# Kernel tuning notes

Measured on AMD Instinct MI355X. Metric: run time of the kernel, lower is better.

The kernel has to match this reference:

```python
import jax, jax.numpy as jnp
import numpy as np

N_EMBD = 2048
H_I = 16   # indexer heads
D_I = 32   # indexer dim


def setup_inputs() -> dict:
    key = jax.random.key(0)
    k1, k2, k3, k4 = jax.random.split(key, 4)
    x = jax.random.normal(k1, (2, 4096, N_EMBD), dtype=jnp.float32)
    # nn.Linear(in, out, bias=False) weights, stored (out, in) like torch
    s = 1.0 / np.sqrt(N_EMBD)
    Wq = jax.random.uniform(k2, (H_I * D_I, N_EMBD), jnp.float32, -s, s)
    Wk = jax.random.uniform(k3, (D_I, N_EMBD), jnp.float32, -s, s)
    Ww = jax.random.uniform(k4, (H_I, N_EMBD), jnp.float32, -s, s)
    return {"x": x, "Wq": Wq, "Wk": Wk, "Ww": Ww}


def reference(x, Wq, Wk, Ww):
    B, T, C = x.shape
    q = (x @ Wq.T).reshape(B, T, H_I, D_I)   # (B,T,H,D)
    k = x @ Wk.T                              # (B,T,D)
    w = x @ Ww.T                              # (B,T,H)
    scores = jnp.einsum('bqhd,bkd->bqhk', q, k)
    scores = jax.nn.relu(scores)
    importance = jnp.einsum('bqh,bqhk->bqk', w, scores)  # (B,T,T)
    return importance
```

## Files before the change

kernel.cpp:

```cpp
#include <hip/hip_runtime.h>
#include <hip/hip_bf16.h>
#include <stdint.h>


typedef __attribute__((ext_vector_type(8))) short bf16x8;
typedef __attribute__((ext_vector_type(4))) float f32x4;
typedef __attribute__((ext_vector_type(2))) __fp16 f16x2;

__device__ __forceinline__ unsigned short f2bf(float f) {
  union { float f; unsigned u; } c; c.f = f;
  unsigned u = c.u;
  u += 0x7FFFu + ((u >> 16) & 1u);
  return (unsigned short)(u >> 16);
}

__device__ __forceinline__ f16x2 u32_to_h2(unsigned u) {
  union { unsigned u; f16x2 h; } c; c.u = u; return c.h;
}
__device__ __forceinline__ unsigned h2_to_u32(f16x2 h) {
  union { unsigned u; f16x2 h; } c; c.h = h; return c.u;
}

__device__ __forceinline__ void async_copy16(void* lds, const void* g) {
  __builtin_amdgcn_global_load_lds(
      (const __attribute__((address_space(1))) unsigned*)g,
      (__attribute__((address_space(3))) unsigned*)lds, 16, 0, 0);
}

__global__ __launch_bounds__(256) void pack_kernel(
    const float* __restrict__ x, const float* __restrict__ Wq,
    const float* __restrict__ Wk, const float* __restrict__ Ww,
    unsigned short* __restrict__ xb, unsigned short* __restrict__ Wp) {
  const int64_t NX4 = 16777216 / 4;
  int64_t i = (int64_t)blockIdx.x * 256 + threadIdx.x;
  if (i < NX4) {
    float4 v = ((const float4*)x)[i];
    ushort4 o;
    o.x = f2bf(v.x); o.y = f2bf(v.y); o.z = f2bf(v.z); o.w = f2bf(v.w);
    ((ushort4*)xb)[i] = o;
  } else {
    int p = (int)(i - NX4);
    int row = p >> 9;
    int col = (p & 511) << 2;
    float4 v = make_float4(0.f, 0.f, 0.f, 0.f);
    if (row < 512)      v = *(const float4*)(Wq + (int64_t)row * 2048 + col);
    else if (row < 544) v = *(const float4*)(Wk + (int64_t)(row - 512) * 2048 + col);
    else if (row < 560) v = *(const float4*)(Ww + (int64_t)(row - 544) * 2048 + col);
    ushort4 o;
    o.x = f2bf(v.x); o.y = f2bf(v.y); o.z = f2bf(v.z); o.w = f2bf(v.w);
    ((ushort4*)Wp)[p] = o;
  }
}

__global__ __launch_bounds__(256) void gemm_proj(
    const unsigned short* __restrict__ xb, const unsigned short* __restrict__ Wp,
    unsigned short* __restrict__ qh, unsigned short* __restrict__ kh,
    float* __restrict__ wf) {
  __shared__ short lds_a[2][64 * 64];
  __shared__ short lds_b[2][128 * 64];
  const int tid = threadIdx.x;
  const int lane = tid & 63;
  const int l15 = lane & 15, quad = lane >> 4;
  const int wave = tid >> 6;
  const int wn = wave;
  const int m0 = blockIdx.y * 64, n0 = blockIdx.x * 128;

  f32x4 acc[4][2] = {};

#define STAGE_A(buf, ko)                                                        \
  {                                                                             \
    _Pragma("unroll") for (int cc = 0; cc < 2; ++cc) {                          \
      int c = tid + cc * 256;                                                   \
      async_copy16(&lds_a[buf][c * 8],                                          \
                   xb + (int64_t)(m0 + (c >> 3)) * 2048 + (ko) + (c & 7) * 8);  \
    }                                                                           \
  }
#define STAGE_B(buf, ko)                                                        \
  {                                                                             \
    _Pragma("unroll") for (int cc = 0; cc < 4; ++cc) {                          \
      int c = tid + cc * 256;                                                   \
      async_copy16(&lds_b[buf][c * 8],                                          \
                   Wp + (int64_t)(n0 + (c >> 3)) * 2048 + (ko) + (c & 7) * 8);  \
    }                                                                           \
  }

  STAGE_A(0, 0);
  STAGE_B(0, 0);
  __syncthreads();

  for (int kt = 0; kt < 32; ++kt) {
    const int cur = kt & 1, nxt = cur ^ 1;
    if (kt < 31) {
      STAGE_A(nxt, (kt + 1) * 64);
      STAGE_B(nxt, (kt + 1) * 64);
    }
    bf16x8 af[4][2], bfr[2][2];
#pragma unroll
    for (int i = 0; i < 4; ++i)
#pragma unroll
      for (int s = 0; s < 2; ++s)
        af[i][s] = *(const bf16x8*)&lds_a[cur][(i * 16 + l15) * 64 + s * 32 + quad * 8];
#pragma unroll
    for (int j = 0; j < 2; ++j)
#pragma unroll
      for (int s = 0; s < 2; ++s)
        bfr[j][s] = *(const bf16x8*)&lds_b[cur][(wn * 32 + j * 16 + l15) * 64 + s * 32 + quad * 8];
#pragma unroll
    for (int s = 0; s < 2; ++s)
#pragma unroll
      for (int i = 0; i < 4; ++i)
#pragma unroll
        for (int j = 0; j < 2; ++j)
          acc[i][j] = __builtin_amdgcn_mfma_f32_16x16x32_bf16(af[i][s], bfr[j][s], acc[i][j], 0, 0, 0);
    __syncthreads();
  }
#undef STAGE_A
#undef STAGE_B

#pragma unroll
  for (int i = 0; i < 4; ++i)
#pragma unroll
    for (int j = 0; j < 2; ++j)
#pragma unroll
      for (int r = 0; r < 4; ++r) {
        int m = m0 + i * 16 + quad * 4 + r;
        int n = n0 + wn * 32 + j * 16 + l15;
        float v = acc[i][j][r];
        if (n < 512)      qh[((int64_t)(n >> 5) * 8192 + m) * 32 + (n & 31)] = f2bf(v);
        else if (n < 544) kh[(int64_t)m * 32 + (n - 512)] = f2bf(v);
        else if (n < 560) wf[m * 16 + (n - 544)] = v;
      }
}

__global__ __launch_bounds__(256) void scores_kernel(
    const unsigned short* __restrict__ qh, const unsigned short* __restrict__ kh,
    const float* __restrict__ wf, float* __restrict__ out) {
  const int kt = blockIdx.x, qt = blockIdx.y, b = blockIdx.z;
  const int tid = threadIdx.x;
  const int lane = tid & 63;
  const int l15 = lane & 15, quad = lane >> 4;
  const int wave = tid >> 6;
  const int wk = wave & 1, wq = wave >> 1;

  __shared__ unsigned w2[8][132];

  const int qrow0 = b * 4096 + qt * 128;
  const int krow0 = b * 4096 + kt * 128;

  {
    const float4* ws = (const float4*)(wf + (int64_t)qrow0 * 16);
#pragma unroll
    for (int r = 0; r < 2; ++r) {
      int f = tid * 2 + r;
      float4 v = ws[f];
      int row = f >> 2, hb = (f & 3) * 4;
      f16x2 p01, p23;
      p01.x = (__fp16)v.x; p01.y = (__fp16)v.y;
      p23.x = (__fp16)v.z; p23.y = (__fp16)v.w;
      w2[(hb >> 1) + 0][row] = h2_to_u32(p01);
      w2[(hb >> 1) + 1][row] = h2_to_u32(p23);
    }
  }

  bf16x8 ka[4];
#pragma unroll
  for (int i = 0; i < 4; ++i) {
    int kk = krow0 + wk * 64 + i * 16 + l15;
    ka[i] = *(const bf16x8*)&kh[(int64_t)kk * 32 + quad * 8];
  }

  const unsigned short* qbase =
      qh + (int64_t)(qrow0 + wq * 64 + l15) * 32 + quad * 8;

  f32x4 acc[4][4] = {};
  __syncthreads();

  const f16x2 hz = u32_to_h2(0u);
  const f32x4 z = {0.f, 0.f, 0.f, 0.f};

#pragma unroll
  for (int hp = 0; hp < 8; ++hp) {
    bf16x8 q0[4], q1[4];
#pragma unroll
    for (int j = 0; j < 4; ++j) {
      q0[j] = *(const bf16x8*)&qbase[(int64_t)(2 * hp) * 262144 + j * 512];
      q1[j] = *(const bf16x8*)&qbase[(int64_t)(2 * hp + 1) * 262144 + j * 512];
    }
    f16x2 wv[4];
#pragma unroll
    for (int j = 0; j < 4; ++j)
      wv[j] = u32_to_h2(w2[hp][wq * 64 + j * 16 + l15]);

#pragma unroll
    for (int i = 0; i < 4; ++i)
#pragma unroll
      for (int j = 0; j < 4; ++j) {
        f32x4 t0 = __builtin_amdgcn_mfma_f32_16x16x32_bf16(ka[i], q0[j], z, 0, 0, 0);
        f32x4 t1 = __builtin_amdgcn_mfma_f32_16x16x32_bf16(ka[i], q1[j], z, 0, 0, 0);
#pragma unroll
        for (int r = 0; r < 4; ++r) {
          f16x2 p = __builtin_amdgcn_cvt_pkrtz(t0[r], t1[r]);
          p = __builtin_elementwise_max(p, hz);
          acc[i][j][r] = __builtin_amdgcn_fdot2(p, wv[j], acc[i][j][r], false);
        }
      }
  }

#pragma unroll
  for (int i = 0; i < 4; ++i)
#pragma unroll
    for (int j = 0; j < 4; ++j) {
      int q = qt * 128 + wq * 64 + j * 16 + l15;
      int k = kt * 128 + wk * 64 + i * 16 + quad * 4;
      float4 v = make_float4(acc[i][j][0], acc[i][j][1], acc[i][j][2], acc[i][j][3]);
      *(float4*)&out[((int64_t)b * 4096 + q) * 4096 + k] = v;
    }
}

extern "C" void kernel_launch(void* const* d_in, const int* in_sizes, int n_in,
                              void* d_out, int out_size, void* d_ws, size_t ws_size,
                              hipStream_t stream) {
  const float* x  = (const float*)d_in[0];
  const float* Wq = (const float*)d_in[1];
  const float* Wk = (const float*)d_in[2];
  const float* Ww = (const float*)d_in[3];
  float* out = (float*)d_out;

  char* ws = (char*)d_ws;
  unsigned short* xb = (unsigned short*)ws;
  unsigned short* Wp = (unsigned short*)(ws + 33554432);
  unsigned short* qh = (unsigned short*)(ws + 36175872);
  unsigned short* kh = (unsigned short*)(ws + 44564480);
  float*          wf = (float*)(ws + 45088768);

  pack_kernel<<<17664, 256, 0, stream>>>(x, Wq, Wk, Ww, xb, Wp);
  gemm_proj<<<dim3(5, 128), 256, 0, stream>>>(xb, Wp, qh, kh, wf);
  scores_kernel<<<dim3(32, 32, 2), 256, 0, stream>>>(qh, kh, wf, out);
}
```

Before: 291.7 us.

## Fuse fp32-to-bf16 conversion of x into projection GEMM A-tile loading

Removes the separate pass that converted all of x to bf16 in workspace; the pack kernel now only converts the weights. The projection GEMM loads fp32 x directly into registers, converts it to bf16, and writes it to LDS after the MFMA work of the current k-step, keeping double buffering. This avoids a full read/write round trip of x, but each of the five N-tile blocks now re-reads fp32 x, doubling bytes per A element and replacing async LDS copies with register staging.

```diff
diff --git a/kernel.cpp b/kernel.cpp
--- a/kernel.cpp
+++ b/kernel.cpp
@@ -27,33 +27,23 @@
       (__attribute__((address_space(3))) unsigned*)lds, 16, 0, 0);
 }
 
-__global__ __launch_bounds__(256) void pack_kernel(
-    const float* __restrict__ x, const float* __restrict__ Wq,
-    const float* __restrict__ Wk, const float* __restrict__ Ww,
-    unsigned short* __restrict__ xb, unsigned short* __restrict__ Wp) {
-  const int64_t NX4 = 16777216 / 4;
-  int64_t i = (int64_t)blockIdx.x * 256 + threadIdx.x;
-  if (i < NX4) {
-    float4 v = ((const float4*)x)[i];
-    ushort4 o;
-    o.x = f2bf(v.x); o.y = f2bf(v.y); o.z = f2bf(v.z); o.w = f2bf(v.w);
-    ((ushort4*)xb)[i] = o;
-  } else {
-    int p = (int)(i - NX4);
-    int row = p >> 9;
-    int col = (p & 511) << 2;
-    float4 v = make_float4(0.f, 0.f, 0.f, 0.f);
-    if (row < 512)      v = *(const float4*)(Wq + (int64_t)row * 2048 + col);
-    else if (row < 544) v = *(const float4*)(Wk + (int64_t)(row - 512) * 2048 + col);
-    else if (row < 560) v = *(const float4*)(Ww + (int64_t)(row - 544) * 2048 + col);
-    ushort4 o;
-    o.x = f2bf(v.x); o.y = f2bf(v.y); o.z = f2bf(v.z); o.w = f2bf(v.w);
-    ((ushort4*)Wp)[p] = o;
-  }
+__global__ __launch_bounds__(256) void packw_kernel(
+    const float* __restrict__ Wq, const float* __restrict__ Wk,
+    const float* __restrict__ Ww, unsigned short* __restrict__ Wp) {
+  int p = blockIdx.x * 256 + threadIdx.x;
+  int row = p >> 9;
+  int col = (p & 511) << 2;
+  float4 v = make_float4(0.f, 0.f, 0.f, 0.f);
+  if (row < 512)      v = *(const float4*)(Wq + (int64_t)row * 2048 + col);
+  else if (row < 544) v = *(const float4*)(Wk + (int64_t)(row - 512) * 2048 + col);
+  else if (row < 560) v = *(const float4*)(Ww + (int64_t)(row - 544) * 2048 + col);
+  ushort4 o;
+  o.x = f2bf(v.x); o.y = f2bf(v.y); o.z = f2bf(v.z); o.w = f2bf(v.w);
+  ((ushort4*)Wp)[p] = o;
 }
 
 __global__ __launch_bounds__(256) void gemm_proj(
-    const unsigned short* __restrict__ xb, const unsigned short* __restrict__ Wp,
+    const float* __restrict__ x, const unsigned short* __restrict__ Wp,
     unsigned short* __restrict__ qh, unsigned short* __restrict__ kh,
     float* __restrict__ wf) {
   __shared__ short lds_a[2][64 * 64];
@@ -65,16 +55,13 @@
   const int wn = wave;
   const int m0 = blockIdx.y * 64, n0 = blockIdx.x * 128;
 
+  const int arow = tid >> 2, acg = tid & 3;
+  const float* gax = x + (int64_t)(m0 + arow) * 2048 + acg * 16;
+  short* lda_dst0 = &lds_a[0][arow * 64 + acg * 16];
+  short* lda_dst1 = &lds_a[1][arow * 64 + acg * 16];
+
   f32x4 acc[4][2] = {};
 
-#define STAGE_A(buf, ko)                                                        \
-  {                                                                             \
-    _Pragma("unroll") for (int cc = 0; cc < 2; ++cc) {                          \
-      int c = tid + cc * 256;                                                   \
-      async_copy16(&lds_a[buf][c * 8],                                          \
-                   xb + (int64_t)(m0 + (c >> 3)) * 2048 + (ko) + (c & 7) * 8);  \
-    }                                                                           \
-  }
 #define STAGE_B(buf, ko)                                                        \
   {                                                                             \
     _Pragma("unroll") for (int cc = 0; cc < 4; ++cc) {                          \
@@ -83,16 +70,43 @@
                    Wp + (int64_t)(n0 + (c >> 3)) * 2048 + (ko) + (c & 7) * 8);  \
     }                                                                           \
   }
-
-  STAGE_A(0, 0);
-  STAGE_B(0, 0);
+#define LOAD_A(ko)                                                              \
+  f32x4 av0 = *(const f32x4*)(gax + (ko));                                      \
+  f32x4 av1 = *(const f32x4*)(gax + (ko) + 4);                                  \
+  f32x4 av2 = *(const f32x4*)(gax + (ko) + 8);                                  \
+  f32x4 av3 = *(const f32x4*)(gax + (ko) + 12);
+#define WRITE_A(dst)                                                            \
+  {                                                                             \
+    bf16x8 w0, w1;                                                              \
+    w0[0] = (short)f2bf(av0[0]); w0[1] = (short)f2bf(av0[1]);                   \
+    w0[2] = (short)f2bf(av0[2]); w0[3] = (short)f2bf(av0[3]);                   \
+    w0[4] = (short)f2bf(av1[0]); w0[5] = (short)f2bf(av1[1]);                   \
+    w0[6] = (short)f2bf(av1[2]); w0[7] = (short)f2bf(av1[3]);                   \
+    w1[0] = (short)f2bf(av2[0]); w1[1] = (short)f2bf(av2[1]);                   \
+    w1[2] = (short)f2bf(av2[2]); w1[3] = (short)f2bf(av2[3]);                   \
+    w1[4] = (short)f2bf(av3[0]); w1[5] = (short)f2bf(av3[1]);                   \
+    w1[6] = (short)f2bf(av3[2]); w1[7] = (short)f2bf(av3[3]);                   \
+    *(bf16x8*)(dst) = w0;                                                       \
+    *(bf16x8*)((dst) + 8) = w1;                                                 \
+  }
+
+  {
+    LOAD_A(0);
+    STAGE_B(0, 0);
+    WRITE_A(lda_dst0);
+  }
   __syncthreads();
 
   for (int kt = 0; kt < 32; ++kt) {
-    const int cur = kt & 1, nxt = cur ^ 1;
+    const int cur = kt & 1;
+    f32x4 av0, av1, av2, av3;
     if (kt < 31) {
-      STAGE_A(nxt, (kt + 1) * 64);
-      STAGE_B(nxt, (kt + 1) * 64);
+      const float* g = gax + (kt + 1) * 64;
+      av0 = *(const f32x4*)(g);
+      av1 = *(const f32x4*)(g + 4);
+      av2 = *(const f32x4*)(g + 8);
+      av3 = *(const f32x4*)(g + 12);
+      STAGE_B(cur ^ 1, (kt + 1) * 64);
     }
     bf16x8 af[4][2], bfr[2][2];
 #pragma unroll
@@ -112,10 +126,15 @@
 #pragma unroll
         for (int j = 0; j < 2; ++j)
           acc[i][j] = __builtin_amdgcn_mfma_f32_16x16x32_bf16(af[i][s], bfr[j][s], acc[i][j], 0, 0, 0);
+    if (kt < 31) {
+      short* dst = (cur ^ 1) ? lda_dst1 : lda_dst0;
+      WRITE_A(dst);
+    }
     __syncthreads();
   }
-#undef STAGE_A
 #undef STAGE_B
+#undef LOAD_A
+#undef WRITE_A
 
 #pragma unroll
   for (int i = 0; i < 4; ++i)
@@ -227,13 +246,12 @@
   float* out = (float*)d_out;
 
   char* ws = (char*)d_ws;
-  unsigned short* xb = (unsigned short*)ws;
-  unsigned short* Wp = (unsigned short*)(ws + 33554432);
-  unsigned short* qh = (unsigned short*)(ws + 36175872);
-  unsigned short* kh = (unsigned short*)(ws + 44564480);
-  float*          wf = (float*)(ws + 45088768);
-
-  pack_kernel<<<17664, 256, 0, stream>>>(x, Wq, Wk, Ww, xb, Wp);
-  gemm_proj<<<dim3(5, 128), 256, 0, stream>>>(xb, Wp, qh, kh, wf);
+  unsigned short* Wp = (unsigned short*)ws;
+  unsigned short* qh = (unsigned short*)(ws + 2621440);
+  unsigned short* kh = (unsigned short*)(ws + 11010048);
+  float*          wf = (float*)(ws + 11534336);
+
+  packw_kernel<<<1280, 256, 0, stream>>>(Wq, Wk, Ww, Wp);
+  gemm_proj<<<dim3(5, 128), 256, 0, stream>>>(x, Wp, qh, kh, wf);
   scores_kernel<<<dim3(32, 32, 2), 256, 0, stream>>>(qh, kh, wf, out);
 }
```

After: 287.1 us. No clear change (-1.6%).
